# Optimization experiments

Measured on AMD Instinct MI355X. Metric: run time of the kernel, lower is better.

The kernel has to match this reference:

```python
import jax, jax.numpy as jnp
import numpy as np

N, E = 50000, 400000
IC, OC, WIDTH, DEPTH = 128, 128, 2, 3


def setup_inputs() -> dict:
    key = jax.random.key(0)
    ks = jax.random.split(key, 9)
    s = 0.02
    return {
        "node_tensor": jax.random.normal(ks[0], (N, 1, IC), jnp.float32),
        "edge_index": jax.random.randint(ks[1], (2, E), 0, N, dtype=jnp.int32),
        "W_pre": jax.random.normal(ks[2], (IC, OC * WIDTH), jnp.float32) * s,
        "b_pre": jax.random.normal(ks[3], (OC * WIDTH,), jnp.float32) * s,
        "W_merge": jax.random.normal(ks[4], (IC, OC * WIDTH), jnp.float32) * s,
        "b_merge": jax.random.normal(ks[5], (OC * WIDTH,), jnp.float32) * s,
        "W_conv": jax.random.normal(ks[6], (WIDTH, OC, OC), jnp.float32) * s,
        "b_conv": jax.random.normal(ks[7], (OC * WIDTH,), jnp.float32) * s,
    }


def reference(node_tensor, edge_index, W_pre, b_pre, W_merge, b_merge, W_conv, b_conv):
    n = node_tensor.shape[0]
    nodes = node_tensor[:, 0, :]                       # (N, IC)

    src, dst = edge_index[0], edge_index[1]
    deg = jax.ops.segment_sum(jnp.ones((E,), node_tensor.dtype), dst, num_segments=n)
    norm = jnp.where(deg > 0, jax.lax.rsqrt(jnp.maximum(deg, 1.0)), 0.0)  # D^{-1/2}

    def laplacian_action(x):                           # x: (N, C); L_sym x
        agg = jax.ops.segment_sum(norm[src, None] * x[src], dst, num_segments=n)
        return x - norm[:, None] * agg

    merge = nodes @ W_merge + b_merge                  # (N, OC*W)
    out = jax.nn.relu(nodes @ W_pre + b_pre + merge)   # (N, OC*W)

    for _ in range(DEPTH - 1):
        out = out - laplacian_action(out)
        # grouped 1x1 conv: width contiguous groups of OC channels
        h = out.reshape(n, WIDTH, OC)
        h = jnp.einsum("nwi,woi->nwo", h, W_conv).reshape(n, WIDTH * OC) + b_conv
        out = jax.nn.relu(h + merge)

    # final (N, OC, W) reshape + adaptive_avg_pool1d(1) == mean over width
    out = out.reshape(n, OC, WIDTH).mean(axis=-1)
    return out[:, :, None]                             # (N, OC, 1)
```

## Files before the change

kernel.cpp:

```cpp
#include <hip/hip_runtime.h>

typedef unsigned short u16;
typedef __attribute__((ext_vector_type(8))) short bf16x8;
typedef __attribute__((ext_vector_type(4))) float f32x4;

#define ICNST 128
#define C2 256

__device__ __forceinline__ float bf2f(u16 u){
  return __uint_as_float(((unsigned int)u) << 16);
}
__device__ __forceinline__ float2 bf2x2(unsigned int u){
  float2 r;
  r.x = __uint_as_float(u << 16);
  r.y = __uint_as_float(u & 0xffff0000u);
  return r;
}
__device__ __forceinline__ u16 f2bf(float f){
  unsigned int u = __float_as_uint(f);
  unsigned int r = (u + 0x7fffu + ((u >> 16) & 1u)) >> 16;
  return (u16)r;
}
__device__ __forceinline__ unsigned int pk2(float a, float b){
  return (unsigned int)f2bf(a) | ((unsigned int)f2bf(b) << 16);
}

__global__ void k_deg(const int* __restrict__ dst, int* __restrict__ deg, int E){
  int e = blockIdx.x * blockDim.x + threadIdx.x;
  if (e < E) atomicAdd(&deg[dst[e]], 1);
}

__global__ __launch_bounds__(256) void k_scan1(const int* __restrict__ deg,
    int* __restrict__ bsum, int n){
  __shared__ int red[256];
  int t = threadIdx.x;
  int i = blockIdx.x * 256 + t;
  red[t] = (i < n) ? deg[i] : 0;
  __syncthreads();
  for (int off = 128; off > 0; off >>= 1){
    if (t < off) red[t] += red[t + off];
    __syncthreads();
  }
  if (t == 0) bsum[blockIdx.x] = red[0];
}

__global__ __launch_bounds__(256) void k_scan2(int* __restrict__ bsum, int nb){
  __shared__ int s[256];
  int t = threadIdx.x;
  int v = (t < nb) ? bsum[t] : 0;
  s[t] = v;
  __syncthreads();
  for (int off = 1; off < 256; off <<= 1){
    int u = (t >= off) ? s[t - off] : 0;
    __syncthreads();
    s[t] += u;
    __syncthreads();
  }
  if (t < nb) bsum[t] = s[t] - v;
}

__global__ __launch_bounds__(256) void k_scan3(const int* __restrict__ deg,
    const int* __restrict__ bsum, int* __restrict__ row_start,
    int* __restrict__ cursor, float* __restrict__ norm, int n){
  __shared__ int s[256];
  int t = threadIdx.x;
  int i = blockIdx.x * 256 + t;
  int v = (i < n) ? deg[i] : 0;
  s[t] = v;
  __syncthreads();
  for (int off = 1; off < 256; off <<= 1){
    int u = (t >= off) ? s[t - off] : 0;
    __syncthreads();
    s[t] += u;
    __syncthreads();
  }
  int ex = s[t] - v + bsum[blockIdx.x];
  if (i < n){
    row_start[i] = ex;
    cursor[i] = ex;
    norm[i] = (v > 0) ? rsqrtf((float)v) : 0.f;
    if (i == n - 1) row_start[n] = ex + v;
  }
}

__global__ void k_scatter(const int* __restrict__ src, const int* __restrict__ dstA,
    int* __restrict__ cursor, int* __restrict__ csr_src, int E){
  int e = blockIdx.x * blockDim.x + threadIdx.x;
  if (e < E){
    int d = dstA[e];
    int pos = atomicAdd(&cursor[d], 1);
    csr_src[pos] = src[e];
  }
}

__global__ void k_cvtW(const float* __restrict__ Wpre, const float* __restrict__ Wmrg,
    const float* __restrict__ Wcv, u16* __restrict__ WT, u16* __restrict__ Wc){
  int idx = blockIdx.x * blockDim.x + threadIdx.x;
  if (idx < 65536){
    int j = idx & 511, k = idx >> 9;
    float v = (j < 256) ? Wpre[k * 256 + j] : Wmrg[k * 256 + (j - 256)];
    WT[j * 128 + k] = f2bf(v);
  } else if (idx < 65536 + 32768){
    int x = idx - 65536;
    Wc[x] = f2bf(Wcv[x]);
  }
}

__global__ __launch_bounds__(512) void k_initM(const float* __restrict__ node,
    const u16* __restrict__ WT, const float* __restrict__ bpre,
    const float* __restrict__ bmrg, const float* __restrict__ norm,
    u16* __restrict__ merge, u16* __restrict__ outA, int n){
  __shared__ u16 Al[64 * 128];
  int t = threadIdx.x;
  int w = t >> 6, l = t & 63;
  int n0 = blockIdx.x * 64;
  int cb = w * 32;

  {
    int row = t >> 3, c0 = (t & 7) * 16;
    const float* src = node + (size_t)(n0 + row) * ICNST + c0;
    bool ok = (n0 + row) < n;
    #pragma unroll
    for (int q = 0; q < 4; ++q){
      float4 v = ok ? *(const float4*)(src + q * 4) : float4{0.f, 0.f, 0.f, 0.f};
      int byte = (row * 256 + c0 * 2 + q * 8) ^ ((row & 7) << 4);
      unsigned int pv = pk2(v.x, v.y);
      unsigned int pw = pk2(v.z, v.w);
      uint2 pp; pp.x = pv; pp.y = pw;
      *(uint2*)((char*)Al + byte) = pp;
    }
  }
  __syncthreads();

  f32x4 acc[4][4] = {};
  int lk = (l >> 4) * 8;
  #pragma unroll
  for (int ks = 0; ks < 4; ++ks){
    bf16x8 bf[4];
    #pragma unroll
    for (int fc = 0; fc < 4; ++fc){
      int j = (fc < 2) ? (cb + fc * 16 + (l & 15))
                       : (256 + cb + (fc - 2) * 16 + (l & 15));
      bf[fc] = *(const bf16x8*)(WT + (size_t)j * 128 + ks * 32 + lk);
    }
    bf16x8 af[4];
    #pragma unroll
    for (int fr = 0; fr < 4; ++fr){
      int row = fr * 16 + (l & 15);
      int byte = (row * 256 + ks * 64 + (l >> 4) * 16) ^ ((l & 7) << 4);
      af[fr] = *(const bf16x8*)((const char*)Al + byte);
    }
    #pragma unroll
    for (int fr = 0; fr < 4; ++fr)
      #pragma unroll
      for (int fc = 0; fc < 4; ++fc)
        acc[fr][fc] = __builtin_amdgcn_mfma_f32_16x16x32_bf16(bf[fc], af[fr], acc[fr][fc], 0, 0, 0);
  }

  #pragma unroll
  for (int fr = 0; fr < 4; ++fr){
    int row = n0 + fr * 16 + (l & 15);
    bool ok = row < n;
    float nr = ok ? norm[row] : 0.f;
    #pragma unroll
    for (int fcp = 0; fcp < 2; ++fcp){
      int j0 = cb + fcp * 16 + (l >> 4) * 4;
      float4 bP = *(const float4*)(bpre + j0);
      float4 bM = *(const float4*)(bmrg + j0);
      f32x4 aP = acc[fr][fcp], aM = acc[fr][fcp + 2];
      float bPe[4] = {bP.x, bP.y, bP.z, bP.w};
      float bMe[4] = {bM.x, bM.y, bM.z, bM.w};
      ushort4 mgv, outv;
      u16* mgp = (u16*)&mgv; u16* otp = (u16*)&outv;
      #pragma unroll
      for (int r = 0; r < 4; ++r){
        float mg = aM[r] + bMe[r];
        float o  = aP[r] + bPe[r] + mg;
        o = (o > 0.f) ? o : 0.f;
        mgp[r] = f2bf(mg);
        otp[r] = f2bf(nr * o);
      }
      if (ok){
        *(ushort4*)(merge + (size_t)row * C2 + j0) = mgv;
        *(ushort4*)(outA  + (size_t)row * C2 + j0) = outv;
      }
    }
  }
}

template<int FINAL>
__global__ __launch_bounds__(512) void k_convM(u16* __restrict__ buf,
    const u16* __restrict__ Wc, const float* __restrict__ bc,
    const u16* __restrict__ merge, const float* __restrict__ norm,
    float* __restrict__ out, int n){
  __shared__ u16 Al[64 * 256];
  int t = threadIdx.x;
  int w = t >> 6, l = t & 63;
  int n0 = blockIdx.x * 64;
  int wh = w >> 2;

  {
    int row = t >> 3, c0 = (t & 7) * 32;
    const u16* src = buf + (size_t)(n0 + row) * C2 + c0;
    bool ok = (n0 + row) < n;
    #pragma unroll
    for (int q = 0; q < 4; ++q){
      uint4 v = ok ? *(const uint4*)(src + q * 8) : uint4{0u, 0u, 0u, 0u};
      int byte = (row * 512 + c0 * 2 + q * 16) ^ ((row & 7) << 4);
      *(uint4*)((char*)Al + byte) = v;
    }
  }
  __syncthreads();

  f32x4 acc[4][2] = {};
  int lk = (l >> 4) * 8;
  #pragma unroll
  for (int ks = 0; ks < 4; ++ks){
    bf16x8 bf[2];
    #pragma unroll
    for (int fc = 0; fc < 2; ++fc){
      int rw = w * 32 + fc * 16 + (l & 15);
      bf[fc] = *(const bf16x8*)(Wc + (size_t)rw * 128 + ks * 32 + lk);
    }
    bf16x8 af[4];
    #pragma unroll
    for (int fr = 0; fr < 4; ++fr){
      int row = fr * 16 + (l & 15);
      int byte = (row * 512 + wh * 256 + ks * 64 + (l >> 4) * 16) ^ ((l & 7) << 4);
      af[fr] = *(const bf16x8*)((const char*)Al + byte);
    }
    #pragma unroll
    for (int fr = 0; fr < 4; ++fr)
      #pragma unroll
      for (int fc = 0; fc < 2; ++fc)
        acc[fr][fc] = __builtin_amdgcn_mfma_f32_16x16x32_bf16(bf[fc], af[fr], acc[fr][fc], 0, 0, 0);
  }

  #pragma unroll
  for (int fr = 0; fr < 4; ++fr){
    int row = n0 + fr * 16 + (l & 15);
    bool ok = row < n;
    float nr = 0.f;
    if (!FINAL) nr = ok ? norm[row] : 0.f;
    #pragma unroll
    for (int fc = 0; fc < 2; ++fc){
      int j0 = w * 32 + fc * 16 + (l >> 4) * 4;
      float4 bC = *(const float4*)(bc + j0);
      float bCe[4] = {bC.x, bC.y, bC.z, bC.w};
      ushort4 mg4 = ok ? *(const ushort4*)(merge + (size_t)row * C2 + j0)
                       : ushort4{0, 0, 0, 0};
      const u16* mge = (const u16*)&mg4;
      float v[4];
      #pragma unroll
      for (int r = 0; r < 4; ++r){
        float o = acc[fr][fc][r] + bCe[r] + bf2f(mge[r]);
        v[r] = (o > 0.f) ? o : 0.f;
      }
      if (!FINAL){
        ushort4 ov;
        u16* ovp = (u16*)&ov;
        #pragma unroll
        for (int r = 0; r < 4; ++r) ovp[r] = f2bf(nr * v[r]);
        if (ok) *(ushort4*)(buf + (size_t)row * C2 + j0) = ov;
      } else {
        float2 om;
        om.x = 0.5f * (v[0] + v[1]);
        om.y = 0.5f * (v[2] + v[3]);
        if (ok) *(float2*)(out + (size_t)row * 128 + (j0 >> 1)) = om;
      }
    }
  }
}

__global__ __launch_bounds__(256) void k_prop(const u16* __restrict__ A, u16* __restrict__ B,
    const int* __restrict__ row_start, const int* __restrict__ csr,
    const float* __restrict__ norm, int n){
  int gw = (blockIdx.x * blockDim.x + threadIdx.x) >> 6;
  int lane = threadIdx.x & 63;
  if (gw >= n) return;
  int b = row_start[gw], e = row_start[gw + 1];
  float a0 = 0.f, a1 = 0.f, a2 = 0.f, a3 = 0.f;
  int j = b;
  for (; j + 4 <= e; j += 4){
    int i0 = csr[j], i1 = csr[j + 1], i2 = csr[j + 2], i3 = csr[j + 3];
    uint2 r0 = *(const uint2*)(A + (size_t)i0 * C2 + lane * 4);
    uint2 r1 = *(const uint2*)(A + (size_t)i1 * C2 + lane * 4);
    uint2 r2 = *(const uint2*)(A + (size_t)i2 * C2 + lane * 4);
    uint2 r3 = *(const uint2*)(A + (size_t)i3 * C2 + lane * 4);
    float2 p;
    p = bf2x2(r0.x); a0 += p.x; a1 += p.y; p = bf2x2(r0.y); a2 += p.x; a3 += p.y;
    p = bf2x2(r1.x); a0 += p.x; a1 += p.y; p = bf2x2(r1.y); a2 += p.x; a3 += p.y;
    p = bf2x2(r2.x); a0 += p.x; a1 += p.y; p = bf2x2(r2.y); a2 += p.x; a3 += p.y;
    p = bf2x2(r3.x); a0 += p.x; a1 += p.y; p = bf2x2(r3.y); a2 += p.x; a3 += p.y;
  }
  for (; j < e; ++j){
    int i0 = csr[j];
    uint2 r0 = *(const uint2*)(A + (size_t)i0 * C2 + lane * 4);
    float2 p;
    p = bf2x2(r0.x); a0 += p.x; a1 += p.y; p = bf2x2(r0.y); a2 += p.x; a3 += p.y;
  }
  float nd = norm[gw];
  ushort4 ov;
  ov.x = f2bf(nd * a0); ov.y = f2bf(nd * a1);
  ov.z = f2bf(nd * a2); ov.w = f2bf(nd * a3);
  *(ushort4*)(B + (size_t)gw * C2 + lane * 4) = ov;
}

extern "C" void kernel_launch(void* const* d_in, const int* in_sizes, int n_in,
                              void* d_out, int out_size, void* d_ws, size_t ws_size,
                              hipStream_t stream){
  const float* node = (const float*)d_in[0];
  const int*   eidx = (const int*)d_in[1];
  const float* Wpre = (const float*)d_in[2];
  const float* bpre = (const float*)d_in[3];
  const float* Wmrg = (const float*)d_in[4];
  const float* bmrg = (const float*)d_in[5];
  const float* Wcv  = (const float*)d_in[6];
  const float* bcv  = (const float*)d_in[7];
  float* out = (float*)d_out;

  const int n = in_sizes[0] / ICNST;
  const int E = in_sizes[1] / 2;
  const int* srcp = eidx;
  const int* dstp = eidx + E;

  char* ws = (char*)d_ws;
  size_t off = 0;
  auto alloc = [&](size_t bytes) -> char* {
    char* p = ws + off;
    off += bytes;
    off = (off + 255) & ~(size_t)255;
    return p;
  };
  int*   deg       = (int*)  alloc((size_t)n * 4);
  float* norm      = (float*)alloc((size_t)n * 4);
  int*   row_start = (int*)  alloc((size_t)(n + 1) * 4);
  int*   cursor    = (int*)  alloc((size_t)n * 4);
  int*   csr       = (int*)  alloc((size_t)E * 4);
  u16*   merge     = (u16*)  alloc((size_t)n * C2 * 2);
  u16*   bufA      = (u16*)  alloc((size_t)n * C2 * 2);
  u16*   bufB      = (u16*)  alloc((size_t)n * C2 * 2);
  u16*   WT        = (u16*)  alloc((size_t)512 * 128 * 2);
  u16*   Wcbf      = (u16*)  alloc((size_t)2 * 128 * 128 * 2);
  int*   bsum      = (int*)  alloc((size_t)256 * 4);
  (void)ws_size; (void)n_in; (void)out_size;

  const int nb = (n + 255) / 256;

  hipMemsetAsync(deg, 0, (size_t)n * 4, stream);
  k_cvtW<<<384, 256, 0, stream>>>(Wpre, Wmrg, Wcv, WT, Wcbf);
  k_deg<<<(E + 255) / 256, 256, 0, stream>>>(dstp, deg, E);
  k_scan1<<<nb, 256, 0, stream>>>(deg, bsum, n);
  k_scan2<<<1, 256, 0, stream>>>(bsum, nb);
  k_scan3<<<nb, 256, 0, stream>>>(deg, bsum, row_start, cursor, norm, n);
  k_scatter<<<(E + 255) / 256, 256, 0, stream>>>(srcp, dstp, cursor, csr, E);

  int gb64 = (n + 63) / 64;
  k_initM<<<gb64, 512, 0, stream>>>(node, WT, bpre, bmrg, norm, merge, bufA, n);

  k_prop<<<(n + 3) / 4, 256, 0, stream>>>(bufA, bufB, row_start, csr, norm, n);
  k_convM<0><<<gb64, 512, 0, stream>>>(bufB, Wcbf, bcv, merge, norm, nullptr, n);
  k_prop<<<(n + 3) / 4, 256, 0, stream>>>(bufB, bufA, row_start, csr, norm, n);
  k_convM<1><<<gb64, 512, 0, stream>>>(bufA, Wcbf, bcv, merge, norm, out, n);
}
```

Before: 215.4 us.

## Fuse weight conversion with degree count, prefetch operands, widen propagation loads

Merges the weight-conversion and degree-atomic kernels into a single launch. In the GEMM kernels, weight fragments, norms, biases and merge values are loaded into registers before the tile load and barrier, so their latency overlaps the shared-memory fill. The propagation kernel now serves two nodes per wavefront, each half using 16-byte loads per neighbor row, which halves the grid. This raises register pressure in the GEMM kernels and may lower occupancy; in the FINAL conv path norm is now read unconditionally.

```diff
diff --git a/kernel.cpp b/kernel.cpp
--- a/kernel.cpp
+++ b/kernel.cpp
@@ -25,9 +25,25 @@
   return (unsigned int)f2bf(a) | ((unsigned int)f2bf(b) << 16);
 }
 
-__global__ void k_deg(const int* __restrict__ dst, int* __restrict__ deg, int E){
-  int e = blockIdx.x * blockDim.x + threadIdx.x;
-  if (e < E) atomicAdd(&deg[dst[e]], 1);
+__global__ __launch_bounds__(256) void k_pre(const int* __restrict__ dst,
+    int* __restrict__ deg, const float* __restrict__ Wpre,
+    const float* __restrict__ Wmrg, const float* __restrict__ Wcv,
+    u16* __restrict__ WT, u16* __restrict__ Wc, int E){
+  int bid = blockIdx.x;
+  if (bid < 384){
+    int idx = bid * 256 + threadIdx.x;
+    if (idx < 65536){
+      int j = idx & 511, k = idx >> 9;
+      float v = (j < 256) ? Wpre[k * 256 + j] : Wmrg[k * 256 + (j - 256)];
+      WT[j * 128 + k] = f2bf(v);
+    } else if (idx < 65536 + 32768){
+      int x = idx - 65536;
+      Wc[x] = f2bf(Wcv[x]);
+    }
+  } else {
+    int e = (bid - 384) * 256 + threadIdx.x;
+    if (e < E) atomicAdd(&deg[dst[e]], 1);
+  }
 }
 
 __global__ __launch_bounds__(256) void k_scan1(const int* __restrict__ deg,
@@ -93,19 +109,6 @@
   }
 }
 
-__global__ void k_cvtW(const float* __restrict__ Wpre, const float* __restrict__ Wmrg,
-    const float* __restrict__ Wcv, u16* __restrict__ WT, u16* __restrict__ Wc){
-  int idx = blockIdx.x * blockDim.x + threadIdx.x;
-  if (idx < 65536){
-    int j = idx & 511, k = idx >> 9;
-    float v = (j < 256) ? Wpre[k * 256 + j] : Wmrg[k * 256 + (j - 256)];
-    WT[j * 128 + k] = f2bf(v);
-  } else if (idx < 65536 + 32768){
-    int x = idx - 65536;
-    Wc[x] = f2bf(Wcv[x]);
-  }
-}
-
 __global__ __launch_bounds__(512) void k_initM(const float* __restrict__ node,
     const u16* __restrict__ WT, const float* __restrict__ bpre,
     const float* __restrict__ bmrg, const float* __restrict__ norm,
@@ -115,6 +118,30 @@
   int w = t >> 6, l = t & 63;
   int n0 = blockIdx.x * 64;
   int cb = w * 32;
+  int lk = (l >> 4) * 8;
+
+  bf16x8 breg[4][4];
+  #pragma unroll
+  for (int ks = 0; ks < 4; ++ks)
+    #pragma unroll
+    for (int fc = 0; fc < 4; ++fc){
+      int j = (fc < 2) ? (cb + fc * 16 + (l & 15))
+                       : (256 + cb + (fc - 2) * 16 + (l & 15));
+      breg[ks][fc] = *(const bf16x8*)(WT + (size_t)j * 128 + ks * 32 + lk);
+    }
+  float nr4[4];
+  #pragma unroll
+  for (int fr = 0; fr < 4; ++fr){
+    int row = n0 + fr * 16 + (l & 15);
+    nr4[fr] = (row < n) ? norm[row] : 0.f;
+  }
+  float4 bPr[2], bMr[2];
+  #pragma unroll
+  for (int fcp = 0; fcp < 2; ++fcp){
+    int j0 = cb + fcp * 16 + (l >> 4) * 4;
+    bPr[fcp] = *(const float4*)(bpre + j0);
+    bMr[fcp] = *(const float4*)(bmrg + j0);
+  }
 
   {
     int row = t >> 3, c0 = (t & 7) * 16;
@@ -124,25 +151,15 @@
     for (int q = 0; q < 4; ++q){
       float4 v = ok ? *(const float4*)(src + q * 4) : float4{0.f, 0.f, 0.f, 0.f};
       int byte = (row * 256 + c0 * 2 + q * 8) ^ ((row & 7) << 4);
-      unsigned int pv = pk2(v.x, v.y);
-      unsigned int pw = pk2(v.z, v.w);
-      uint2 pp; pp.x = pv; pp.y = pw;
+      uint2 pp; pp.x = pk2(v.x, v.y); pp.y = pk2(v.z, v.w);
       *(uint2*)((char*)Al + byte) = pp;
     }
   }
   __syncthreads();
 
   f32x4 acc[4][4] = {};
-  int lk = (l >> 4) * 8;
   #pragma unroll
   for (int ks = 0; ks < 4; ++ks){
-    bf16x8 bf[4];
-    #pragma unroll
-    for (int fc = 0; fc < 4; ++fc){
-      int j = (fc < 2) ? (cb + fc * 16 + (l & 15))
-                       : (256 + cb + (fc - 2) * 16 + (l & 15));
-      bf[fc] = *(const bf16x8*)(WT + (size_t)j * 128 + ks * 32 + lk);
-    }
     bf16x8 af[4];
     #pragma unroll
     for (int fr = 0; fr < 4; ++fr){
@@ -154,22 +171,20 @@
     for (int fr = 0; fr < 4; ++fr)
       #pragma unroll
       for (int fc = 0; fc < 4; ++fc)
-        acc[fr][fc] = __builtin_amdgcn_mfma_f32_16x16x32_bf16(bf[fc], af[fr], acc[fr][fc], 0, 0, 0);
+        acc[fr][fc] = __builtin_amdgcn_mfma_f32_16x16x32_bf16(breg[ks][fc], af[fr], acc[fr][fc], 0, 0, 0);
   }
 
   #pragma unroll
   for (int fr = 0; fr < 4; ++fr){
     int row = n0 + fr * 16 + (l & 15);
     bool ok = row < n;
-    float nr = ok ? norm[row] : 0.f;
+    float nr = nr4[fr];
     #pragma unroll
     for (int fcp = 0; fcp < 2; ++fcp){
       int j0 = cb + fcp * 16 + (l >> 4) * 4;
-      float4 bP = *(const float4*)(bpre + j0);
-      float4 bM = *(const float4*)(bmrg + j0);
       f32x4 aP = acc[fr][fcp], aM = acc[fr][fcp + 2];
-      float bPe[4] = {bP.x, bP.y, bP.z, bP.w};
-      float bMe[4] = {bM.x, bM.y, bM.z, bM.w};
+      float bPe[4] = {bPr[fcp].x, bPr[fcp].y, bPr[fcp].z, bPr[fcp].w};
+      float bMe[4] = {bMr[fcp].x, bMr[fcp].y, bMr[fcp].z, bMr[fcp].w};
       ushort4 mgv, outv;
       u16* mgp = (u16*)&mgv; u16* otp = (u16*)&outv;
       #pragma unroll
@@ -198,6 +213,38 @@
   int w = t >> 6, l = t & 63;
   int n0 = blockIdx.x * 64;
   int wh = w >> 2;
+  int lk = (l >> 4) * 8;
+
+  bf16x8 breg[4][2];
+  #pragma unroll
+  for (int ks = 0; ks < 4; ++ks)
+    #pragma unroll
+    for (int fc = 0; fc < 2; ++fc){
+      int rw = w * 32 + fc * 16 + (l & 15);
+      breg[ks][fc] = *(const bf16x8*)(Wc + (size_t)rw * 128 + ks * 32 + lk);
+    }
+  float nr4[4];
+  #pragma unroll
+  for (int fr = 0; fr < 4; ++fr){
+    int row = n0 + fr * 16 + (l & 15);
+    nr4[fr] = (row < n) ? norm[row] : 0.f;
+  }
+  float4 bCr[2];
+  ushort4 mgr[4][2];
+  #pragma unroll
+  for (int fc = 0; fc < 2; ++fc)
+    bCr[fc] = *(const float4*)(bc + w * 32 + fc * 16 + (l >> 4) * 4);
+  #pragma unroll
+  for (int fr = 0; fr < 4; ++fr){
+    int row = n0 + fr * 16 + (l & 15);
+    bool ok = row < n;
+    #pragma unroll
+    for (int fc = 0; fc < 2; ++fc){
+      int j0 = w * 32 + fc * 16 + (l >> 4) * 4;
+      mgr[fr][fc] = ok ? *(const ushort4*)(merge + (size_t)row * C2 + j0)
+                       : ushort4{0, 0, 0, 0};
+    }
+  }
 
   {
     int row = t >> 3, c0 = (t & 7) * 32;
@@ -213,15 +260,8 @@
   __syncthreads();
 
   f32x4 acc[4][2] = {};
-  int lk = (l >> 4) * 8;
   #pragma unroll
   for (int ks = 0; ks < 4; ++ks){
-    bf16x8 bf[2];
-    #pragma unroll
-    for (int fc = 0; fc < 2; ++fc){
-      int rw = w * 32 + fc * 16 + (l & 15);
-      bf[fc] = *(const bf16x8*)(Wc + (size_t)rw * 128 + ks * 32 + lk);
-    }
     bf16x8 af[4];
     #pragma unroll
     for (int fr = 0; fr < 4; ++fr){
@@ -233,23 +273,19 @@
     for (int fr = 0; fr < 4; ++fr)
       #pragma unroll
       for (int fc = 0; fc < 2; ++fc)
-        acc[fr][fc] = __builtin_amdgcn_mfma_f32_16x16x32_bf16(bf[fc], af[fr], acc[fr][fc], 0, 0, 0);
+        acc[fr][fc] = __builtin_amdgcn_mfma_f32_16x16x32_bf16(breg[ks][fc], af[fr], acc[fr][fc], 0, 0, 0);
   }
 
   #pragma unroll
   for (int fr = 0; fr < 4; ++fr){
     int row = n0 + fr * 16 + (l & 15);
     bool ok = row < n;
-    float nr = 0.f;
-    if (!FINAL) nr = ok ? norm[row] : 0.f;
+    float nr = nr4[fr];
     #pragma unroll
     for (int fc = 0; fc < 2; ++fc){
       int j0 = w * 32 + fc * 16 + (l >> 4) * 4;
-      float4 bC = *(const float4*)(bc + j0);
-      float bCe[4] = {bC.x, bC.y, bC.z, bC.w};
-      ushort4 mg4 = ok ? *(const ushort4*)(merge + (size_t)row * C2 + j0)
-                       : ushort4{0, 0, 0, 0};
-      const u16* mge = (const u16*)&mg4;
+      float bCe[4] = {bCr[fc].x, bCr[fc].y, bCr[fc].z, bCr[fc].w};
+      const u16* mge = (const u16*)&mgr[fr][fc];
       float v[4];
       #pragma unroll
       for (int r = 0; r < 4; ++r){
@@ -275,35 +311,45 @@
 __global__ __launch_bounds__(256) void k_prop(const u16* __restrict__ A, u16* __restrict__ B,
     const int* __restrict__ row_start, const int* __restrict__ csr,
     const float* __restrict__ norm, int n){
-  int gw = (blockIdx.x * blockDim.x + threadIdx.x) >> 6;
+  int wid = (blockIdx.x * 256 + threadIdx.x) >> 6;
   int lane = threadIdx.x & 63;
+  int half = lane >> 5, c = lane & 31;
+  int gw = wid * 2 + half;
   if (gw >= n) return;
   int b = row_start[gw], e = row_start[gw + 1];
-  float a0 = 0.f, a1 = 0.f, a2 = 0.f, a3 = 0.f;
+  float a0 = 0.f, a1 = 0.f, a2 = 0.f, a3 = 0.f, a4 = 0.f, a5 = 0.f, a6 = 0.f, a7 = 0.f;
+  const u16* Ac = A + (size_t)c * 8;
   int j = b;
   for (; j + 4 <= e; j += 4){
-    int i0 = csr[j], i1 = csr[j + 1], i2 = csr[j + 2], i3 = csr[j + 3];
-    uint2 r0 = *(const uint2*)(A + (size_t)i0 * C2 + lane * 4);
-    uint2 r1 = *(const uint2*)(A + (size_t)i1 * C2 + lane * 4);
-    uint2 r2 = *(const uint2*)(A + (size_t)i2 * C2 + lane * 4);
-    uint2 r3 = *(const uint2*)(A + (size_t)i3 * C2 + lane * 4);
+    int s0 = csr[j], s1 = csr[j + 1], s2 = csr[j + 2], s3 = csr[j + 3];
+    uint4 r0 = *(const uint4*)(Ac + (size_t)s0 * C2);
+    uint4 r1 = *(const uint4*)(Ac + (size_t)s1 * C2);
+    uint4 r2 = *(const uint4*)(Ac + (size_t)s2 * C2);
+    uint4 r3 = *(const uint4*)(Ac + (size_t)s3 * C2);
     float2 p;
     p = bf2x2(r0.x); a0 += p.x; a1 += p.y; p = bf2x2(r0.y); a2 += p.x; a3 += p.y;
+    p = bf2x2(r0.z); a4 += p.x; a5 += p.y; p = bf2x2(r0.w); a6 += p.x; a7 += p.y;
     p = bf2x2(r1.x); a0 += p.x; a1 += p.y; p = bf2x2(r1.y); a2 += p.x; a3 += p.y;
+    p = bf2x2(r1.z); a4 += p.x; a5 += p.y; p = bf2x2(r1.w); a6 += p.x; a7 += p.y;
     p = bf2x2(r2.x); a0 += p.x; a1 += p.y; p = bf2x2(r2.y); a2 += p.x; a3 += p.y;
+    p = bf2x2(r2.z); a4 += p.x; a5 += p.y; p = bf2x2(r2.w); a6 += p.x; a7 += p.y;
     p = bf2x2(r3.x); a0 += p.x; a1 += p.y; p = bf2x2(r3.y); a2 += p.x; a3 += p.y;
+    p = bf2x2(r3.z); a4 += p.x; a5 += p.y; p = bf2x2(r3.w); a6 += p.x; a7 += p.y;
   }
   for (; j < e; ++j){
-    int i0 = csr[j];
-    uint2 r0 = *(const uint2*)(A + (size_t)i0 * C2 + lane * 4);
+    int s0 = csr[j];
+    uint4 r0 = *(const uint4*)(Ac + (size_t)s0 * C2);
     float2 p;
     p = bf2x2(r0.x); a0 += p.x; a1 += p.y; p = bf2x2(r0.y); a2 += p.x; a3 += p.y;
+    p = bf2x2(r0.z); a4 += p.x; a5 += p.y; p = bf2x2(r0.w); a6 += p.x; a7 += p.y;
   }
   float nd = norm[gw];
-  ushort4 ov;
-  ov.x = f2bf(nd * a0); ov.y = f2bf(nd * a1);
-  ov.z = f2bf(nd * a2); ov.w = f2bf(nd * a3);
-  *(ushort4*)(B + (size_t)gw * C2 + lane * 4) = ov;
+  uint4 ov;
+  ov.x = pk2(nd * a0, nd * a1);
+  ov.y = pk2(nd * a2, nd * a3);
+  ov.z = pk2(nd * a4, nd * a5);
+  ov.w = pk2(nd * a6, nd * a7);
+  *(uint4*)(B + (size_t)gw * C2 + c * 8) = ov;
 }
 
 extern "C" void kernel_launch(void* const* d_in, const int* in_sizes, int n_in,
@@ -348,8 +394,7 @@
   const int nb = (n + 255) / 256;
 
   hipMemsetAsync(deg, 0, (size_t)n * 4, stream);
-  k_cvtW<<<384, 256, 0, stream>>>(Wpre, Wmrg, Wcv, WT, Wcbf);
-  k_deg<<<(E + 255) / 256, 256, 0, stream>>>(dstp, deg, E);
+  k_pre<<<384 + (E + 255) / 256, 256, 0, stream>>>(dstp, deg, Wpre, Wmrg, Wcv, WT, Wcbf, E);
   k_scan1<<<nb, 256, 0, stream>>>(deg, bsum, n);
   k_scan2<<<1, 256, 0, stream>>>(bsum, nb);
   k_scan3<<<nb, 256, 0, stream>>>(deg, bsum, row_start, cursor, norm, n);
@@ -358,8 +403,8 @@
   int gb64 = (n + 63) / 64;
   k_initM<<<gb64, 512, 0, stream>>>(node, WT, bpre, bmrg, norm, merge, bufA, n);
 
-  k_prop<<<(n + 3) / 4, 256, 0, stream>>>(bufA, bufB, row_start, csr, norm, n);
+  k_prop<<<(n + 7) / 8, 256, 0, stream>>>(bufA, bufB, row_start, csr, norm, n);
   k_convM<0><<<gb64, 512, 0, stream>>>(bufB, Wcbf, bcv, merge, norm, nullptr, n);
-  k_prop<<<(n + 3) / 4, 256, 0, stream>>>(bufB, bufA, row_start, csr, norm, n);
+  k_prop<<<(n + 7) / 8, 256, 0, stream>>>(bufB, bufA, row_start, csr, norm, n);
   k_convM<1><<<gb64, 512, 0, stream>>>(bufA, Wcbf, bcv, merge, norm, out, n);
 }
```

Result: no change. 214.9 us (-0.2%).
